# Optimization experiments

Measured on AMD Instinct MI355X. Metric: run time of the kernel, lower is better.

The kernel has to match this reference:

```python
import jax, jax.numpy as jnp
import numpy as np

B, S, E, H = 4, 2048, 1024, 16
K = 9           # number of boundaries per batch (K-1 = 8 passages)
DH = E // H


def make_relevance_mask(boundaries, relevance_scores, seq_len):
    """Vectorized equivalent of the Python-loop mask builder.

    boundaries: (B, K) int, sorted; boundaries[:,0] == q_end.
    relevance_scores: (B, K-1) float.
    Returns float mask (B, S, S) with values {0, 1, relevance}.
    """
    Bsz, Kb = boundaries.shape
    idx = jnp.arange(seq_len, dtype=boundaries.dtype)
    # pid[b, s] = j s.t. boundaries[b, j] <= s < boundaries[b, j+1]; -1 before b[0]
    pid = jax.vmap(lambda bb: jnp.searchsorted(bb, idx, side='right'))(boundaries) - 1  # (B,S)
    in_pass = (pid >= 0) & (pid < Kb - 1)  # inside some passage span
    rel_g = jnp.take_along_axis(relevance_scores, jnp.clip(pid, 0, Kb - 2), axis=1)  # (B,S)
    # query rows (pos < q_end): columns in passage j -> relevance[j], else 1
    col_val = jnp.where(in_pass, rel_g, 1.0)  # (B,S)
    qrow = idx[None, :] < boundaries[:, :1]   # (B,S)
    # non-query rows: 1 iff same passage block, else 0
    same = in_pass[:, :, None] & in_pass[:, None, :] & (pid[:, :, None] == pid[:, None, :])
    mask = jnp.where(qrow[:, :, None], col_val[:, None, :], jnp.where(same, 1.0, 0.0))
    return mask.astype(jnp.float32)


def setup_inputs() -> dict:
    key = jax.random.key(0)
    k1, k2, k3, k4, k5, k6, k7 = jax.random.split(key, 7)
    hidden_states = jax.random.normal(k1, (B, S, E), dtype=jnp.float32)
    relevance_scores = jax.random.uniform(k2, (B, K - 1), dtype=jnp.float32)
    passage_boundaries = jnp.sort(jax.random.randint(k3, (B, K), 0, S, dtype=jnp.int32), axis=1)
    in_proj_w = 0.02 * jax.random.normal(k4, (3 * E, E), dtype=jnp.float32)
    in_proj_b = jnp.zeros((3 * E,), dtype=jnp.float32)
    out_w = 0.02 * jax.random.normal(k5, (E, E), dtype=jnp.float32)
    out_b = jnp.zeros((E,), dtype=jnp.float32)
    return {
        'hidden_states': hidden_states,
        'relevance_scores': relevance_scores,
        'passage_boundaries': passage_boundaries,
        'in_proj_w': in_proj_w,
        'in_proj_b': in_proj_b,
        'out_w': out_w,
        'out_b': out_b,
    }


def reference(hidden_states, relevance_scores, passage_boundaries,
              in_proj_w, in_proj_b, out_w, out_b):
    Bsz, Sl, Em = hidden_states.shape
    mask = make_relevance_mask(passage_boundaries, relevance_scores, Sl)  # (B,S,S)
    qkv = hidden_states @ in_proj_w.T + in_proj_b              # (B,S,3E)
    q, k, v = jnp.split(qkv, 3, axis=-1)
    def heads(t):
        return t.reshape(Bsz, Sl, H, DH).transpose(0, 2, 1, 3)  # (B,H,S,Dh)
    q, k, v = heads(q), heads(k), heads(v)
    scale = 1.0 / jnp.sqrt(jnp.float32(DH))
    scores = jnp.einsum('bhqd,bhkd->bhqk', q * scale, k) + mask[:, None]  # float mask is ADDED
    attn = jax.nn.softmax(scores, axis=-1)
    out = jnp.einsum('bhqk,bhkd->bhqd', attn, v)
    out = out.transpose(0, 2, 1, 3).reshape(Bsz, Sl, Em)
    return out @ out_w.T + out_b
```

## Files before the change

### kernel.cpp

```cpp
#include <hip/hip_runtime.h>
#include <math.h>

#define Bsz 4
#define Sq  2048
#define Eq  1024
#define Hh  16
#define DHd 64
#define Kb  9
#define STR 72
#define GSTR 72

typedef _Float16 f16;
typedef __attribute__((ext_vector_type(8))) _Float16 fh8;
typedef __attribute__((ext_vector_type(4))) float fx4;

__global__ void pid_kernel(const int* __restrict__ bnd, const float* __restrict__ rel,
                           int* __restrict__ pidq, float* __restrict__ colval) {
  int idx = blockIdx.x * blockDim.x + threadIdx.x;
  if (idx >= Bsz * Sq) return;
  int b = idx >> 11;
  int s = idx & (Sq - 1);
  int j = -1;
#pragma unroll
  for (int t = 0; t < Kb; ++t) {
    if (bnd[b * Kb + t] <= s) j = t;
  }
  pidq[idx] = j;
  colval[idx] = (j >= 0 && j < Kb - 1) ? rel[b * (Kb - 1) + j] : 1.0f;
}

__global__ __launch_bounds__(256) void cvt_hs(const float* __restrict__ x,
                                              f16* __restrict__ xo) {
  int i = (blockIdx.x * blockDim.x + threadIdx.x) * 8;
  float4 a = *(const float4*)&x[i];
  float4 b = *(const float4*)&x[i + 4];
  fh8 o;
  o[0] = (f16)a.x; o[1] = (f16)a.y; o[2] = (f16)a.z; o[3] = (f16)a.w;
  o[4] = (f16)b.x; o[5] = (f16)b.y; o[6] = (f16)b.z; o[7] = (f16)b.w;
  *(fh8*)&xo[i] = o;
}

template <int MODE>
__global__ __launch_bounds__(256) void gemm_f16(
    const f16* __restrict__ A, const float* __restrict__ Bf,
    const float* __restrict__ bias, float* __restrict__ Cp,
    int M, int N, int Kd,
    f16* __restrict__ qo, f16* __restrict__ ko, f16* __restrict__ vto) {
  __shared__ __align__(16) f16 Ash[128 * GSTR];
  __shared__ __align__(16) f16 Bsh[128 * GSTR];

  const int tid = threadIdx.x;
  const int lane = tid & 63, w = tid >> 6;
  const int wm = w >> 1, wn = w & 1;
  const int q16 = lane & 15, quad = lane >> 4;
  const int m_blk = blockIdx.y * 128, n_blk = blockIdx.x * 128;

  fx4 acc[4][4];
#pragma unroll
  for (int mt = 0; mt < 4; ++mt)
#pragma unroll
    for (int nt = 0; nt < 4; ++nt)
#pragma unroll
      for (int r = 0; r < 4; ++r) acc[mt][nt][r] = 0.f;

  const int sr = tid >> 2, sc = (tid & 3) * 16;

  for (int k0 = 0; k0 < Kd; k0 += 64) {
    __syncthreads();
#pragma unroll
    for (int h = 0; h < 2; ++h) {
      const int r = sr + h * 64;
      const f16* ga = &A[(size_t)(m_blk + r) * Kd + k0 + sc];
      *(fh8*)&Ash[r * GSTR + sc]     = *(const fh8*)&ga[0];
      *(fh8*)&Ash[r * GSTR + sc + 8] = *(const fh8*)&ga[8];
      const float* gb = &Bf[(size_t)(n_blk + r) * Kd + k0 + sc];
      float4 f0 = *(const float4*)&gb[0];
      float4 f1 = *(const float4*)&gb[4];
      float4 f2 = *(const float4*)&gb[8];
      float4 f3 = *(const float4*)&gb[12];
      fh8 b0, b1;
      b0[0] = (f16)f0.x; b0[1] = (f16)f0.y; b0[2] = (f16)f0.z; b0[3] = (f16)f0.w;
      b0[4] = (f16)f1.x; b0[5] = (f16)f1.y; b0[6] = (f16)f1.z; b0[7] = (f16)f1.w;
      b1[0] = (f16)f2.x; b1[1] = (f16)f2.y; b1[2] = (f16)f2.z; b1[3] = (f16)f2.w;
      b1[4] = (f16)f3.x; b1[5] = (f16)f3.y; b1[6] = (f16)f3.z; b1[7] = (f16)f3.w;
      *(fh8*)&Bsh[r * GSTR + sc]     = b0;
      *(fh8*)&Bsh[r * GSTR + sc + 8] = b1;
    }
    __syncthreads();

#pragma unroll
    for (int ks = 0; ks < 2; ++ks) {
      fh8 af[4], bfr[4];
#pragma unroll
      for (int mt = 0; mt < 4; ++mt)
        af[mt] = *(const fh8*)&Ash[(wm * 64 + mt * 16 + q16) * GSTR + ks * 32 + quad * 8];
#pragma unroll
      for (int nt = 0; nt < 4; ++nt)
        bfr[nt] = *(const fh8*)&Bsh[(wn * 64 + nt * 16 + q16) * GSTR + ks * 32 + quad * 8];
#pragma unroll
      for (int nt = 0; nt < 4; ++nt)
#pragma unroll
        for (int mt = 0; mt < 4; ++mt)
          acc[mt][nt] = __builtin_amdgcn_mfma_f32_16x16x32_f16(af[mt], bfr[nt], acc[mt][nt], 0, 0, 0);
    }
  }

  float bsv[4];
#pragma unroll
  for (int nt = 0; nt < 4; ++nt) bsv[nt] = bias[n_blk + wn * 64 + nt * 16 + q16];

  if (MODE == 0) {
#pragma unroll
    for (int mt = 0; mt < 4; ++mt)
#pragma unroll
      for (int r = 0; r < 4; ++r) {
        int row = m_blk + wm * 64 + mt * 16 + quad * 4 + r;
#pragma unroll
        for (int nt = 0; nt < 4; ++nt) {
          int col = n_blk + wn * 64 + nt * 16 + q16;
          Cp[(size_t)row * N + col] = acc[mt][nt][r] + bsv[nt];
        }
      }
  } else {
    const int n0 = n_blk + wn * 64;
    const int which = n0 >> 10;
    const int hd = (n0 & 1023) >> 6;
    const float scale = (which == 0) ? 0.125f : 1.0f;
#pragma unroll
    for (int mt = 0; mt < 4; ++mt)
#pragma unroll
      for (int r = 0; r < 4; ++r) {
        int m = m_blk + wm * 64 + mt * 16 + quad * 4 + r;
        int b = m >> 11, s = m & (Sq - 1);
#pragma unroll
        for (int nt = 0; nt < 4; ++nt) {
          int d = nt * 16 + q16;
          float x = (acc[mt][nt][r] + bsv[nt]) * scale;
          if (which == 2) {
            vto[(((size_t)(b * Hh + hd)) * DHd + d) * Sq + s] = (f16)x;
          } else {
            f16* dst = (which == 0) ? qo : ko;
            dst[(((size_t)(b * Hh + hd)) * Sq + s) * DHd + d] = (f16)x;
          }
        }
      }
  }
}

__global__ __launch_bounds__(256, 3) void attn_f16(
    const f16* __restrict__ Qf, const f16* __restrict__ Kf,
    const f16* __restrict__ Vt, const int* __restrict__ pidq,
    const float* __restrict__ colval, f16* __restrict__ attf) {
  const int qb = blockIdx.x, hd = blockIdx.y, b = blockIdx.z;
  const int bh = b * Hh + hd;
  const int tid = threadIdx.x, lane = tid & 63, w = tid >> 6;
  const int q16 = lane & 15, quad = lane >> 4;

  __shared__ __align__(16) f16 Ks[64 * STR];
  __shared__ __align__(16) f16 Vs[64 * STR];
  __shared__ __align__(16) f16 Ps[4][32 * STR];

  const size_t qkbase = (size_t)bh * Sq * DHd;
  const size_t vtbase = (size_t)bh * DHd * Sq;

  fh8 qf[2][2];
#pragma unroll
  for (int mt = 0; mt < 2; ++mt)
#pragma unroll
    for (int ks = 0; ks < 2; ++ks)
      qf[mt][ks] = *(const fh8*)&Qf[qkbase +
          (size_t)(qb * 128 + w * 32 + mt * 16 + q16) * DHd + ks * 32 + quad * 8];

  int pq[8];
#pragma unroll
  for (int mt = 0; mt < 2; ++mt)
#pragma unroll
    for (int r = 0; r < 4; ++r)
      pq[mt * 4 + r] = pidq[b * Sq + qb * 128 + w * 32 + mt * 16 + quad * 4 + r];

  fh8 onesf;
#pragma unroll
  for (int j = 0; j < 8; ++j) onesf[j] = (q16 == 0) ? (f16)1.0f : (f16)0.0f;

  fx4 o_acc[2][4], lacc[2];
#pragma unroll
  for (int mt = 0; mt < 2; ++mt) {
#pragma unroll
    for (int r = 0; r < 4; ++r) lacc[mt][r] = 0.f;
#pragma unroll
    for (int dt = 0; dt < 4; ++dt)
#pragma unroll
      for (int r = 0; r < 4; ++r) o_acc[mt][dt][r] = 0.f;
  }

  for (int kt = 0; kt < 32; ++kt) {
    __syncthreads();
    {
      int n = tid >> 2, c = (tid & 3) * 16;
      size_t gk = qkbase + (size_t)(kt * 64 + n) * DHd + c;
      *(fh8*)&Ks[n * STR + c]     = *(const fh8*)&Kf[gk];
      *(fh8*)&Ks[n * STR + c + 8] = *(const fh8*)&Kf[gk + 8];
      size_t gv = vtbase + (size_t)n * Sq + kt * 64 + c;
      *(fh8*)&Vs[n * STR + c]     = *(const fh8*)&Vt[gv];
      *(fh8*)&Vs[n * STR + c + 8] = *(const fh8*)&Vt[gv + 8];
    }
    __syncthreads();

    fx4 sacc[2][4];
#pragma unroll
    for (int mt = 0; mt < 2; ++mt)
#pragma unroll
      for (int nt = 0; nt < 4; ++nt)
#pragma unroll
        for (int r = 0; r < 4; ++r) sacc[mt][nt][r] = 0.f;

#pragma unroll
    for (int ks = 0; ks < 2; ++ks)
#pragma unroll
      for (int nt = 0; nt < 4; ++nt) {
        fh8 kf8 = *(const fh8*)&Ks[(nt * 16 + q16) * STR + ks * 32 + quad * 8];
#pragma unroll
        for (int mt = 0; mt < 2; ++mt)
          sacc[mt][nt] = __builtin_amdgcn_mfma_f32_16x16x32_f16(qf[mt][ks], kf8, sacc[mt][nt], 0, 0, 0);
      }

    int pcm[4]; float cv[4];
#pragma unroll
    for (int nt = 0; nt < 4; ++nt) {
      int c = kt * 64 + nt * 16 + q16;
      int p = pidq[b * Sq + c];
      pcm[nt] = (p >= 0 && p < Kb - 1) ? p : -2;
      cv[nt] = colval[b * Sq + c];
    }

#pragma unroll
    for (int mt = 0; mt < 2; ++mt)
#pragma unroll
      for (int nt = 0; nt < 4; ++nt)
#pragma unroll
        for (int r = 0; r < 4; ++r) {
          int rq = pq[mt * 4 + r];
          float mv = (rq < 0) ? cv[nt] : ((rq == pcm[nt]) ? 1.0f : 0.0f);
          float p = __expf(sacc[mt][nt][r] + mv);
          Ps[w][(mt * 16 + quad * 4 + r) * STR + nt * 16 + q16] = (f16)p;
        }

#pragma unroll
    for (int ks2 = 0; ks2 < 2; ++ks2) {
      fh8 pf[2];
#pragma unroll
      for (int mt = 0; mt < 2; ++mt)
        pf[mt] = *(const fh8*)&Ps[w][(mt * 16 + q16) * STR + ks2 * 32 + quad * 8];
#pragma unroll
      for (int mt = 0; mt < 2; ++mt)
        lacc[mt] = __builtin_amdgcn_mfma_f32_16x16x32_f16(pf[mt], onesf, lacc[mt], 0, 0, 0);
#pragma unroll
      for (int dt = 0; dt < 4; ++dt) {
        fh8 vf = *(const fh8*)&Vs[(dt * 16 + q16) * STR + ks2 * 32 + quad * 8];
#pragma unroll
        for (int mt = 0; mt < 2; ++mt)
          o_acc[mt][dt] = __builtin_amdgcn_mfma_f32_16x16x32_f16(pf[mt], vf, o_acc[mt][dt], 0, 0, 0);
      }
    }
  }

#pragma unroll
  for (int mt = 0; mt < 2; ++mt)
#pragma unroll
    for (int r = 0; r < 4; ++r) {
      float l = __shfl(lacc[mt][r], (lane >> 4) << 4);
      float inv = 1.0f / l;
      int qg = qb * 128 + w * 32 + mt * 16 + quad * 4 + r;
      size_t base = ((size_t)(b * Sq + qg)) * Eq + hd * 64;
#pragma unroll
      for (int dt = 0; dt < 4; ++dt)
        attf[base + dt * 16 + q16] = (f16)(o_acc[mt][dt][r] * inv);
    }
}

extern "C" void kernel_launch(void* const* d_in, const int* in_sizes, int n_in,
                              void* d_out, int out_size, void* d_ws, size_t ws_size,
                              hipStream_t stream) {
  const float* hs = (const float*)d_in[0];
  const float* rel = (const float*)d_in[1];
  const int* bnd = (const int*)d_in[2];
  const float* wi = (const float*)d_in[3];
  const float* bi = (const float*)d_in[4];
  const float* wo = (const float*)d_in[5];
  const float* bo = (const float*)d_in[6];
  float* out = (float*)d_out;

  const size_t NQ = (size_t)Bsz * Hh * Sq * DHd;
  char* p = (char*)d_ws;
  f16* qf = (f16*)p;   p += NQ * 2;
  f16* kf = (f16*)p;   p += NQ * 2;
  f16* vt = (f16*)p;   p += NQ * 2;
  f16* hsf = (f16*)p;  p += NQ * 2;
  f16* attf = (f16*)p; p += NQ * 2;
  int* pidq = (int*)p; p += Bsz * Sq * 4;
  float* colv = (float*)p;

  hipLaunchKernelGGL(pid_kernel, dim3((Bsz * Sq + 255) / 256), dim3(256), 0, stream,
                     bnd, rel, pidq, colv);
  hipLaunchKernelGGL(cvt_hs, dim3((int)(NQ / 8 / 256)), dim3(256), 0, stream,
                     hs, hsf);
  hipLaunchKernelGGL((gemm_f16<1>), dim3(24, 64), dim3(256), 0, stream,
                     hsf, wi, bi, (float*)nullptr, Bsz * Sq, 3 * Eq, Eq,
                     qf, kf, vt);
  hipLaunchKernelGGL(attn_f16, dim3(16, 16, 4), dim3(256), 0, stream,
                     qf, kf, vt, pidq, colv, attf);
  hipLaunchKernelGGL((gemm_f16<0>), dim3(8, 64), dim3(256), 0, stream,
                     attf, wo, bo, out, Bsz * Sq, Eq, Eq,
                     nullptr, nullptr, nullptr);
}
```

Measured before the change: 364.0 us.

## Rewrite attention with 32x32 MFMA, register-resident P, and exp2 mask factoring

Replaces the LDS-tiled attention kernel with a register-only version built on 32x32x16 MFMA. It computes S^T = K·Q so the P tile can be repacked in registers through permlane32 swaps instead of a shared-memory round trip, and it loads K and V straight from global memory with K prefetched one tile ahead. The additive mask becomes a multiplicative factor exp(mask), precomputed per column, and log2(e) is folded into the Q scale so exp2f can be used. This removes LDS traffic and barriers but relies on L1/L2 reuse of K/V across the four waves and lowers the occupancy hint to 2 blocks.

After: 557.2 us. 1.53x slower.

```diff
diff --git a/kernel.cpp b/kernel.cpp
--- a/kernel.cpp
+++ b/kernel.cpp
@@ -7,15 +7,21 @@
 #define Hh  16
 #define DHd 64
 #define Kb  9
-#define STR 72
 #define GSTR 72
 
 typedef _Float16 f16;
 typedef __attribute__((ext_vector_type(8))) _Float16 fh8;
+typedef __attribute__((ext_vector_type(4))) _Float16 fh4;
+typedef __attribute__((ext_vector_type(2))) _Float16 fh2;
 typedef __attribute__((ext_vector_type(4))) float fx4;
+typedef __attribute__((ext_vector_type(16))) float fx16;
+typedef __attribute__((ext_vector_type(4))) int i4;
+
+#define CE 2.71828182845904523536f
 
 __global__ void pid_kernel(const int* __restrict__ bnd, const float* __restrict__ rel,
-                           int* __restrict__ pidq, float* __restrict__ colval) {
+                           int* __restrict__ pidr, int* __restrict__ pcs,
+                           float* __restrict__ ecv) {
   int idx = blockIdx.x * blockDim.x + threadIdx.x;
   if (idx >= Bsz * Sq) return;
   int b = idx >> 11;
@@ -25,8 +31,11 @@
   for (int t = 0; t < Kb; ++t) {
     if (bnd[b * Kb + t] <= s) j = t;
   }
-  pidq[idx] = j;
-  colval[idx] = (j >= 0 && j < Kb - 1) ? rel[b * (Kb - 1) + j] : 1.0f;
+  pidr[idx] = j;
+  bool inp = (j >= 0 && j < Kb - 1);
+  pcs[idx] = inp ? j : -2;
+  float cv = inp ? rel[b * (Kb - 1) + j] : 1.0f;
+  ecv[idx] = __expf(cv);
 }
 
 __global__ __launch_bounds__(256) void cvt_hs(const float* __restrict__ x,
@@ -125,7 +134,7 @@
     const int n0 = n_blk + wn * 64;
     const int which = n0 >> 10;
     const int hd = (n0 & 1023) >> 6;
-    const float scale = (which == 0) ? 0.125f : 1.0f;
+    const float scale = (which == 0) ? 0.125f * 1.44269504088896340736f : 1.0f;
 #pragma unroll
     for (int mt = 0; mt < 4; ++mt)
 #pragma unroll
@@ -147,134 +156,128 @@
   }
 }
 
-__global__ __launch_bounds__(256, 3) void attn_f16(
+__global__ __launch_bounds__(256, 2) void attn_v2(
     const f16* __restrict__ Qf, const f16* __restrict__ Kf,
-    const f16* __restrict__ Vt, const int* __restrict__ pidq,
-    const float* __restrict__ colval, f16* __restrict__ attf) {
+    const f16* __restrict__ Vt, const int* __restrict__ pidr,
+    const int* __restrict__ pcs, const float* __restrict__ ecv,
+    f16* __restrict__ attf) {
   const int qb = blockIdx.x, hd = blockIdx.y, b = blockIdx.z;
   const int bh = b * Hh + hd;
-  const int tid = threadIdx.x, lane = tid & 63, w = tid >> 6;
-  const int q16 = lane & 15, quad = lane >> 4;
-
-  __shared__ __align__(16) f16 Ks[64 * STR];
-  __shared__ __align__(16) f16 Vs[64 * STR];
-  __shared__ __align__(16) f16 Ps[4][32 * STR];
+  const int tid = threadIdx.x;
+  const int lane = tid & 63, w = tid >> 6;
+  const int l31 = lane & 31, hi = lane >> 5;
 
   const size_t qkbase = (size_t)bh * Sq * DHd;
   const size_t vtbase = (size_t)bh * DHd * Sq;
-
-  fh8 qf[2][2];
-#pragma unroll
-  for (int mt = 0; mt < 2; ++mt)
-#pragma unroll
-    for (int ks = 0; ks < 2; ++ks)
-      qf[mt][ks] = *(const fh8*)&Qf[qkbase +
-          (size_t)(qb * 128 + w * 32 + mt * 16 + q16) * DHd + ks * 32 + quad * 8];
-
-  int pq[8];
-#pragma unroll
-  for (int mt = 0; mt < 2; ++mt)
-#pragma unroll
-    for (int r = 0; r < 4; ++r)
-      pq[mt * 4 + r] = pidq[b * Sq + qb * 128 + w * 32 + mt * 16 + quad * 4 + r];
+  const int qrow = qb * 128 + w * 32 + l31;
+
+  fh8 qf[4];
+  {
+    const f16* qp = &Qf[qkbase + (size_t)qrow * DHd + hi * 8];
+#pragma unroll
+    for (int ds = 0; ds < 4; ++ds) qf[ds] = *(const fh8*)&qp[ds * 16];
+  }
+
+  const int rq = pidr[b * Sq + qrow];
+  const bool isq = (rq < 0);
 
   fh8 onesf;
 #pragma unroll
-  for (int j = 0; j < 8; ++j) onesf[j] = (q16 == 0) ? (f16)1.0f : (f16)0.0f;
-
-  fx4 o_acc[2][4], lacc[2];
-#pragma unroll
-  for (int mt = 0; mt < 2; ++mt) {
-#pragma unroll
-    for (int r = 0; r < 4; ++r) lacc[mt][r] = 0.f;
-#pragma unroll
-    for (int dt = 0; dt < 4; ++dt)
-#pragma unroll
-      for (int r = 0; r < 4; ++r) o_acc[mt][dt][r] = 0.f;
-  }
-
-  for (int kt = 0; kt < 32; ++kt) {
-    __syncthreads();
+  for (int j = 0; j < 8; ++j) onesf[j] = (l31 == 0) ? (f16)1.0f : (f16)0.0f;
+
+  fx16 o_acc[2], lacc;
+#pragma unroll
+  for (int r = 0; r < 16; ++r) { o_acc[0][r] = 0.f; o_acc[1][r] = 0.f; lacc[r] = 0.f; }
+
+  fh8 kf[4];
+  {
+    const f16* kp = &Kf[qkbase + (size_t)l31 * DHd + hi * 8];
+#pragma unroll
+    for (int ds = 0; ds < 4; ++ds) kf[ds] = *(const fh8*)&kp[ds * 16];
+  }
+
+  for (int kt = 0; kt < Sq / 32; ++kt) {
+    fh8 vf[2][2];
+#pragma unroll
+    for (int dt = 0; dt < 2; ++dt)
+#pragma unroll
+      for (int kb = 0; kb < 2; ++kb)
+        vf[dt][kb] = *(const fh8*)&Vt[vtbase + (size_t)(dt * 32 + l31) * Sq +
+                                      kt * 32 + kb * 16 + hi * 8];
+
+    float ec[16]; int pc[16];
     {
-      int n = tid >> 2, c = (tid & 3) * 16;
-      size_t gk = qkbase + (size_t)(kt * 64 + n) * DHd + c;
-      *(fh8*)&Ks[n * STR + c]     = *(const fh8*)&Kf[gk];
-      *(fh8*)&Ks[n * STR + c + 8] = *(const fh8*)&Kf[gk + 8];
-      size_t gv = vtbase + (size_t)n * Sq + kt * 64 + c;
-      *(fh8*)&Vs[n * STR + c]     = *(const fh8*)&Vt[gv];
-      *(fh8*)&Vs[n * STR + c + 8] = *(const fh8*)&Vt[gv + 8];
-    }
-    __syncthreads();
-
-    fx4 sacc[2][4];
-#pragma unroll
-    for (int mt = 0; mt < 2; ++mt)
-#pragma unroll
-      for (int nt = 0; nt < 4; ++nt)
-#pragma unroll
-        for (int r = 0; r < 4; ++r) sacc[mt][nt][r] = 0.f;
-
-#pragma unroll
-    for (int ks = 0; ks < 2; ++ks)
-#pragma unroll
-      for (int nt = 0; nt < 4; ++nt) {
-        fh8 kf8 = *(const fh8*)&Ks[(nt * 16 + q16) * STR + ks * 32 + quad * 8];
-#pragma unroll
-        for (int mt = 0; mt < 2; ++mt)
-          sacc[mt][nt] = __builtin_amdgcn_mfma_f32_16x16x32_f16(qf[mt][ks], kf8, sacc[mt][nt], 0, 0, 0);
+      const int cb = b * Sq + kt * 32 + 4 * hi;
+#pragma unroll
+      for (int g = 0; g < 4; ++g) {
+        float4 e4 = *(const float4*)&ecv[cb + 8 * g];
+        i4 p4 = *(const i4*)&pcs[cb + 8 * g];
+        ec[4 * g + 0] = e4.x; ec[4 * g + 1] = e4.y;
+        ec[4 * g + 2] = e4.z; ec[4 * g + 3] = e4.w;
+        pc[4 * g + 0] = p4[0]; pc[4 * g + 1] = p4[1];
+        pc[4 * g + 2] = p4[2]; pc[4 * g + 3] = p4[3];
       }
-
-    int pcm[4]; float cv[4];
-#pragma unroll
-    for (int nt = 0; nt < 4; ++nt) {
-      int c = kt * 64 + nt * 16 + q16;
-      int p = pidq[b * Sq + c];
-      pcm[nt] = (p >= 0 && p < Kb - 1) ? p : -2;
-      cv[nt] = colval[b * Sq + c];
-    }
-
-#pragma unroll
-    for (int mt = 0; mt < 2; ++mt)
-#pragma unroll
-      for (int nt = 0; nt < 4; ++nt)
-#pragma unroll
-        for (int r = 0; r < 4; ++r) {
-          int rq = pq[mt * 4 + r];
-          float mv = (rq < 0) ? cv[nt] : ((rq == pcm[nt]) ? 1.0f : 0.0f);
-          float p = __expf(sacc[mt][nt][r] + mv);
-          Ps[w][(mt * 16 + quad * 4 + r) * STR + nt * 16 + q16] = (f16)p;
-        }
-
-#pragma unroll
-    for (int ks2 = 0; ks2 < 2; ++ks2) {
-      fh8 pf[2];
-#pragma unroll
-      for (int mt = 0; mt < 2; ++mt)
-        pf[mt] = *(const fh8*)&Ps[w][(mt * 16 + q16) * STR + ks2 * 32 + quad * 8];
-#pragma unroll
-      for (int mt = 0; mt < 2; ++mt)
-        lacc[mt] = __builtin_amdgcn_mfma_f32_16x16x32_f16(pf[mt], onesf, lacc[mt], 0, 0, 0);
-#pragma unroll
-      for (int dt = 0; dt < 4; ++dt) {
-        fh8 vf = *(const fh8*)&Vs[(dt * 16 + q16) * STR + ks2 * 32 + quad * 8];
-#pragma unroll
-        for (int mt = 0; mt < 2; ++mt)
-          o_acc[mt][dt] = __builtin_amdgcn_mfma_f32_16x16x32_f16(pf[mt], vf, o_acc[mt][dt], 0, 0, 0);
-      }
-    }
-  }
-
-#pragma unroll
-  for (int mt = 0; mt < 2; ++mt)
-#pragma unroll
-    for (int r = 0; r < 4; ++r) {
-      float l = __shfl(lacc[mt][r], (lane >> 4) << 4);
-      float inv = 1.0f / l;
-      int qg = qb * 128 + w * 32 + mt * 16 + quad * 4 + r;
-      size_t base = ((size_t)(b * Sq + qg)) * Eq + hd * 64;
-#pragma unroll
-      for (int dt = 0; dt < 4; ++dt)
-        attf[base + dt * 16 + q16] = (f16)(o_acc[mt][dt][r] * inv);
+    }
+
+    fx16 sacc;
+#pragma unroll
+    for (int r = 0; r < 16; ++r) sacc[r] = 0.f;
+#pragma unroll
+    for (int ds = 0; ds < 4; ++ds)
+      sacc = __builtin_amdgcn_mfma_f32_32x32x16_f16(kf[ds], qf[ds], sacc, 0, 0, 0);
+
+    if (kt + 1 < Sq / 32) {
+      const f16* kp = &Kf[qkbase + (size_t)((kt + 1) * 32 + l31) * DHd + hi * 8];
+#pragma unroll
+      for (int ds = 0; ds < 4; ++ds) kf[ds] = *(const fh8*)&kp[ds * 16];
+    }
+
+    float p[16];
+#pragma unroll
+    for (int r = 0; r < 16; ++r) {
+      float f = isq ? ec[r] : ((rq == pc[r]) ? CE : 1.0f);
+      p[r] = exp2f(sacc[r]) * f;
+    }
+    int pk[8];
+#pragma unroll
+    for (int i = 0; i < 8; ++i) {
+      fh2 h; h[0] = (f16)p[2 * i]; h[1] = (f16)p[2 * i + 1];
+      pk[i] = __builtin_bit_cast(int, h);
+    }
+
+#pragma unroll
+    for (int kb = 0; kb < 2; ++kb) {
+      int a01 = pk[4 * kb + 0], a23 = pk[4 * kb + 1];
+      int a45 = pk[4 * kb + 2], a67 = pk[4 * kb + 3];
+      i4 t;
+#if __has_builtin(__builtin_amdgcn_permlane32_swap)
+      auto s0 = __builtin_amdgcn_permlane32_swap(a01, a45, false, false);
+      auto s1 = __builtin_amdgcn_permlane32_swap(a23, a67, false, false);
+      t[0] = s0[0]; t[1] = s1[0]; t[2] = s0[1]; t[3] = s1[1];
+#else
+      int x01 = __shfl_xor(a01, 32), x23 = __shfl_xor(a23, 32);
+      int x45 = __shfl_xor(a45, 32), x67 = __shfl_xor(a67, 32);
+      t[0] = hi ? x45 : a01; t[1] = hi ? x67 : a23;
+      t[2] = hi ? a45 : x01; t[3] = hi ? a67 : x23;
+#endif
+      fh8 pf = __builtin_bit_cast(fh8, t);
+      lacc = __builtin_amdgcn_mfma_f32_32x32x16_f16(onesf, pf, lacc, 0, 0, 0);
+      o_acc[0] = __builtin_amdgcn_mfma_f32_32x32x16_f16(vf[0][kb], pf, o_acc[0], 0, 0, 0);
+      o_acc[1] = __builtin_amdgcn_mfma_f32_32x32x16_f16(vf[1][kb], pf, o_acc[1], 0, 0, 0);
+    }
+  }
+
+  float l = __shfl(lacc[0], l31);
+  float inv = 1.0f / l;
+  size_t obase = ((size_t)(b * Sq + qrow)) * Eq + hd * 64 + 4 * hi;
+#pragma unroll
+  for (int dt = 0; dt < 2; ++dt)
+#pragma unroll
+    for (int g = 0; g < 4; ++g) {
+      fh4 o4;
+#pragma unroll
+      for (int j = 0; j < 4; ++j) o4[j] = (f16)(o_acc[dt][4 * g + j] * inv);
+      *(fh4*)&attf[obase + dt * 32 + 8 * g] = o4;
     }
 }
 
@@ -297,18 +300,19 @@
   f16* vt = (f16*)p;   p += NQ * 2;
   f16* hsf = (f16*)p;  p += NQ * 2;
   f16* attf = (f16*)p; p += NQ * 2;
-  int* pidq = (int*)p; p += Bsz * Sq * 4;
-  float* colv = (float*)p;
+  int* pidr = (int*)p; p += Bsz * Sq * 4;
+  int* pcs = (int*)p;  p += Bsz * Sq * 4;
+  float* ecv = (float*)p;
 
   hipLaunchKernelGGL(pid_kernel, dim3((Bsz * Sq + 255) / 256), dim3(256), 0, stream,
-                     bnd, rel, pidq, colv);
+                     bnd, rel, pidr, pcs, ecv);
   hipLaunchKernelGGL(cvt_hs, dim3((int)(NQ / 8 / 256)), dim3(256), 0, stream,
                      hs, hsf);
   hipLaunchKernelGGL((gemm_f16<1>), dim3(24, 64), dim3(256), 0, stream,
                      hsf, wi, bi, (float*)nullptr, Bsz * Sq, 3 * Eq, Eq,
                      qf, kf, vt);
-  hipLaunchKernelGGL(attn_f16, dim3(16, 16, 4), dim3(256), 0, stream,
-                     qf, kf, vt, pidq, colv, attf);
+  hipLaunchKernelGGL(attn_v2, dim3(16, 16, 4), dim3(256), 0, stream,
+                     qf, kf, vt, pidr, pcs, ecv, attf);
   hipLaunchKernelGGL((gemm_f16<0>), dim3(8, 64), dim3(256), 0, stream,
                      attf, wo, bo, out, Bsz * Sq, Eq, Eq,
                      nullptr, nullptr, nullptr);
```
